# Kernel tuning notes

Measured on AMD Instinct MI355X. Metric: run time of the kernel, lower is better.

The kernel has to match this reference:

```python
import jax, jax.numpy as jnp
import numpy as np

V = 1000      # output_dim (vocab)
H = 512       # hidden_dim
D = 512       # input_dim == d_model of MHA
HEADS = 8
DK = D // HEADS
MEM = 512     # memory_len
BS = 128      # batch
TMAX = 160    # max decode steps (== max(output_lens))


def setup_inputs() -> dict:
    key = jax.random.key(0)
    ks = jax.random.split(key, 16)
    s = 0.05
    f = lambda k, shape: jax.random.normal(k, shape, jnp.float32) * s
    memory = jax.random.normal(ks[0], (MEM, BS, D), jnp.float32)
    lens = jnp.sort(jax.random.randint(ks[1], (BS,), 1, TMAX + 1))[::-1]
    lens = lens.at[0].set(TMAX)  # torch runs max(output_lens) steps; pin to TMAX
    return dict(
        memory=memory,
        emb=f(ks[2], (V, H)),
        Wq=f(ks[3], (D, 2 * H)), bq=f(ks[4], (D,)),
        Wk=f(ks[5], (D, D)), bk=f(ks[6], (D,)),
        Wv=f(ks[7], (D, D)), bv=f(ks[8], (D,)),
        W_ih=f(ks[9], (3 * H, D)), W_hh=f(ks[10], (3 * H, H)),
        b_ih=f(ks[11], (3 * H,)), b_hh=f(ks[12], (3 * H,)),
        Wfc=f(ks[13], (V, H)), bfc=f(ks[14], (V,)),
        output_lens=lens,
    )


def _forward(memory, emb, Wq, bq, Wk, bk, Wv, bv, W_ih, W_hh, b_ih, b_hh, Wfc, bfc, output_lens):
    mem_len, bs, _ = memory.shape
    scale = 1.0 / np.sqrt(DK)
    # Precompute key/value projections once (memory is constant over decode steps).
    # (mem_len, bs, D) -> (bs, heads, mem_len, dk)
    kp = (memory @ Wk.T + bk).reshape(mem_len, bs, HEADS, DK).transpose(1, 2, 0, 3)
    vp = (memory @ Wv.T + bv).reshape(mem_len, bs, HEADS, DK).transpose(1, 2, 0, 3)

    def step(carry, i):
        out, hid = carry  # (bs, V), (bs, H)
        tok = jnp.argmax(out, axis=-1)                 # greedy feedback (annotations=None)
        q = jnp.concatenate([emb[tok], hid], axis=-1) @ Wq.T + bq  # (bs, D)
        qh = q.reshape(bs, HEADS, DK)
        att = jax.nn.softmax(jnp.einsum('bhd,bhmd->bhm', qh, kp) * scale, axis=-1)
        ctx = jnp.einsum('bhm,bhmd->bhd', att, vp).reshape(bs, D)
        # GRU cell (PyTorch gate order: r, z, n)
        gi = ctx @ W_ih.T + b_ih
        gh = hid @ W_hh.T + b_hh
        ir, iz, inn = jnp.split(gi, 3, axis=-1)
        hr, hz, hn = jnp.split(gh, 3, axis=-1)
        r = jax.nn.sigmoid(ir + hr)
        z = jax.nn.sigmoid(iz + hz)
        n = jnp.tanh(inn + r * hn)
        h_new = (1.0 - z) * n + z * hid
        o_new = h_new @ Wfc.T + bfc
        # Ragged masking: torch truncates finished batch items; each item is
        # independent, so masking the recorded outputs is equivalent.
        run = (i < output_lens)[:, None]
        ys = (jnp.where(run, o_new, 0.0),
              jnp.where(run, h_new, 0.0),
              jnp.where(run, att.mean(axis=1), 0.0))
        return (o_new, h_new), ys

    init = (jnp.zeros((bs, V), jnp.float32), jnp.zeros((bs, H), jnp.float32))
    _, (outputs, hiddens, scores) = jax.lax.scan(step, init, jnp.arange(TMAX))
    return outputs, hiddens, scores  # (T,bs,V), (T,bs,H), (T,bs,mem_len)


def reference(memory, emb, Wq, bq, Wk, bk, Wv, bv, W_ih, W_hh, b_ih, b_hh, Wfc, bfc, output_lens):
    return _forward(memory, emb, Wq, bq, Wk, bk, Wv, bv, W_ih, W_hh, b_ih, b_hh, Wfc, bfc, output_lens)
```

## Files before the change

kernel.cpp:

```cpp
#include <hip/hip_runtime.h>
#include <math.h>

__global__ __launch_bounds__(256) void kv_proj(
    const float* __restrict__ mem, const float* __restrict__ W,
    const float* __restrict__ bias, float* __restrict__ outp) {
  __shared__ float As[32][68];
  __shared__ float Bs[32][68];
  int gid = blockIdx.x;
  int jt = gid & 7, mt = (gid >> 3) & 7, b = gid >> 6;
  int t = threadIdx.x;
  int lm = t >> 2;
  int kq = (t & 3) * 8;
  int tx = t & 15, ty = t >> 4;
  float acc[4][4];
  #pragma unroll
  for (int r = 0; r < 4; ++r)
    #pragma unroll
    for (int c = 0; c < 4; ++c) acc[r][c] = 0.f;
  const float* Arow = mem + (size_t)(mt * 64 + lm) * 65536 + (size_t)b * 512 + kq;
  const float* Brow = W + (size_t)(jt * 64 + lm) * 512 + kq;
  for (int k0 = 0; k0 < 512; k0 += 32) {
    float4 a0 = *(const float4*)(Arow + k0);
    float4 a1 = *(const float4*)(Arow + k0 + 4);
    float4 b0 = *(const float4*)(Brow + k0);
    float4 b1 = *(const float4*)(Brow + k0 + 4);
    As[kq + 0][lm] = a0.x; As[kq + 1][lm] = a0.y; As[kq + 2][lm] = a0.z; As[kq + 3][lm] = a0.w;
    As[kq + 4][lm] = a1.x; As[kq + 5][lm] = a1.y; As[kq + 6][lm] = a1.z; As[kq + 7][lm] = a1.w;
    Bs[kq + 0][lm] = b0.x; Bs[kq + 1][lm] = b0.y; Bs[kq + 2][lm] = b0.z; Bs[kq + 3][lm] = b0.w;
    Bs[kq + 4][lm] = b1.x; Bs[kq + 5][lm] = b1.y; Bs[kq + 6][lm] = b1.z; Bs[kq + 7][lm] = b1.w;
    __syncthreads();
    #pragma unroll
    for (int k = 0; k < 32; ++k) {
      float4 av = *(const float4*)&As[k][ty * 4];
      float4 bv = *(const float4*)&Bs[k][tx * 4];
      float ar[4] = {av.x, av.y, av.z, av.w};
      float br[4] = {bv.x, bv.y, bv.z, bv.w};
      #pragma unroll
      for (int r = 0; r < 4; ++r)
        #pragma unroll
        for (int c = 0; c < 4; ++c) acc[r][c] = fmaf(ar[r], br[c], acc[r][c]);
    }
    __syncthreads();
  }
  float4 bb = *(const float4*)(bias + jt * 64 + tx * 4);
  #pragma unroll
  for (int r = 0; r < 4; ++r) {
    int m = mt * 64 + ty * 4 + r;
    float4 o;
    o.x = acc[r][0] + bb.x; o.y = acc[r][1] + bb.y;
    o.z = acc[r][2] + bb.z; o.w = acc[r][3] + bb.w;
    *(float4*)(outp + (((size_t)b * 8 + jt) * 512 + m) * 64 + tx * 4) = o;
  }
}

__global__ __launch_bounds__(256) void kv_projT(
    const float* __restrict__ mem, const float* __restrict__ W,
    const float* __restrict__ bias, float* __restrict__ outp) {
  __shared__ float As[32][68];
  __shared__ float Bs[32][68];
  int gid = blockIdx.x;
  int jt = gid & 7, mt = (gid >> 3) & 7, b = gid >> 6;
  int t = threadIdx.x;
  int lm = t >> 2;
  int kq = (t & 3) * 8;
  int tx = t & 15, ty = t >> 4;
  float acc[4][4];
  #pragma unroll
  for (int r = 0; r < 4; ++r)
    #pragma unroll
    for (int c = 0; c < 4; ++c) acc[r][c] = 0.f;
  const float* Arow = mem + (size_t)(mt * 64 + lm) * 65536 + (size_t)b * 512 + kq;
  const float* Brow = W + (size_t)(jt * 64 + lm) * 512 + kq;
  for (int k0 = 0; k0 < 512; k0 += 32) {
    float4 a0 = *(const float4*)(Arow + k0);
    float4 a1 = *(const float4*)(Arow + k0 + 4);
    float4 b0 = *(const float4*)(Brow + k0);
    float4 b1 = *(const float4*)(Brow + k0 + 4);
    As[kq + 0][lm] = a0.x; As[kq + 1][lm] = a0.y; As[kq + 2][lm] = a0.z; As[kq + 3][lm] = a0.w;
    As[kq + 4][lm] = a1.x; As[kq + 5][lm] = a1.y; As[kq + 6][lm] = a1.z; As[kq + 7][lm] = a1.w;
    Bs[kq + 0][lm] = b0.x; Bs[kq + 1][lm] = b0.y; Bs[kq + 2][lm] = b0.z; Bs[kq + 3][lm] = b0.w;
    Bs[kq + 4][lm] = b1.x; Bs[kq + 5][lm] = b1.y; Bs[kq + 6][lm] = b1.z; Bs[kq + 7][lm] = b1.w;
    __syncthreads();
    #pragma unroll
    for (int k = 0; k < 32; ++k) {
      float4 av = *(const float4*)&As[k][ty * 4];
      float4 bv = *(const float4*)&Bs[k][tx * 4];
      float ar[4] = {av.x, av.y, av.z, av.w};
      float br[4] = {bv.x, bv.y, bv.z, bv.w};
      #pragma unroll
      for (int r = 0; r < 4; ++r)
        #pragma unroll
        for (int c = 0; c < 4; ++c) acc[r][c] = fmaf(ar[r], br[c], acc[r][c]);
    }
    __syncthreads();
  }
  float4 bb = *(const float4*)(bias + jt * 64 + tx * 4);
  float bc[4] = {bb.x, bb.y, bb.z, bb.w};
  #pragma unroll
  for (int r = 0; r < 4; ++r) {
    int m = mt * 64 + ty * 4 + r;
    #pragma unroll
    for (int c = 0; c < 4; ++c) {
      int d = tx * 4 + c;
      outp[((size_t)(b * 8 + jt) * 64 + d) * 512 + m] = acc[r][c] + bc[c];
    }
  }
}

__global__ __launch_bounds__(256) void init_kernel(float* __restrict__ h0,
                                                   unsigned long long* __restrict__ packed) {
  int t = threadIdx.x + blockIdx.x * blockDim.x;
  for (int i = t; i < 128 * 512; i += blockDim.x * gridDim.x) h0[i] = 0.f;
  if (t < 128) packed[t] = (0x80000000ull << 32) | 0xFFFFFFFFull;
}

__global__ __launch_bounds__(256) void attn_fused(
    const float* __restrict__ kpT, const float* __restrict__ vp,
    const float* __restrict__ emb, const float* __restrict__ Wq,
    const float* __restrict__ bq, const unsigned long long* __restrict__ packed,
    const float* __restrict__ h_prev, float* __restrict__ ctx,
    float* __restrict__ att_buf) {
  int b = blockIdx.x >> 3, hd = blockIdx.x & 7;
  __shared__ float act[1024];
  __shared__ float qs[64];
  __shared__ float att[512];
  __shared__ __align__(16) float red[16][68];
  __shared__ float rmax[4], rsum[4];
  __shared__ int tok_s;
  int t = threadIdx.x;
  if (t == 0) tok_s = (int)(0xFFFFFFFFu - (unsigned int)(packed[b] & 0xFFFFFFFFull));
  __syncthreads();
  int tok = tok_s;
  act[t]       = emb[(size_t)tok * 512 + t];
  act[256 + t] = emb[(size_t)tok * 512 + 256 + t];
  act[512 + t] = h_prev[(size_t)b * 512 + t];
  act[768 + t] = h_prev[(size_t)b * 512 + 256 + t];
  __syncthreads();

  {
    int jl = t >> 2, kc = t & 3;
    const float* wrow = Wq + (size_t)(hd * 64 + jl) * 1024 + kc * 256;
    const float* a = act + kc * 256;
    float p = 0.f;
    #pragma unroll 8
    for (int i = 0; i < 256; i += 4) {
      float4 w = *(const float4*)(wrow + i);
      p = fmaf(a[i + 0], w.x, p);
      p = fmaf(a[i + 1], w.y, p);
      p = fmaf(a[i + 2], w.z, p);
      p = fmaf(a[i + 3], w.w, p);
    }
    p += __shfl_xor(p, 1);
    p += __shfl_xor(p, 2);
    if (kc == 0) qs[jl] = p + bq[hd * 64 + jl];
  }
  __syncthreads();

  const float* Kb = kpT + (size_t)(b * 8 + hd) * 32768;
  float s0 = 0.f, s1 = 0.f;
  {
    int m2 = 2 * t;
    #pragma unroll 8
    for (int d = 0; d < 64; ++d) {
      float2 kk = *(const float2*)(Kb + (size_t)d * 512 + m2);
      float qd = qs[d];
      s0 = fmaf(qd, kk.x, s0);
      s1 = fmaf(qd, kk.y, s1);
    }
    s0 *= 0.125f;
    s1 *= 0.125f;
  }
  float mx = fmaxf(s0, s1);
  #pragma unroll
  for (int o = 32; o > 0; o >>= 1) mx = fmaxf(mx, __shfl_xor(mx, o));
  if ((t & 63) == 0) rmax[t >> 6] = mx;
  __syncthreads();
  mx = fmaxf(fmaxf(rmax[0], rmax[1]), fmaxf(rmax[2], rmax[3]));
  float e0 = expf(s0 - mx), e1 = expf(s1 - mx);
  float sm = e0 + e1;
  #pragma unroll
  for (int o = 32; o > 0; o >>= 1) sm += __shfl_xor(sm, o);
  if ((t & 63) == 0) rsum[t >> 6] = sm;
  __syncthreads();
  sm = rsum[0] + rsum[1] + rsum[2] + rsum[3];
  float inv = 1.f / sm;
  float a0 = e0 * inv, a1 = e1 * inv;
  att[2 * t] = a0;
  att[2 * t + 1] = a1;
  *(float2*)(att_buf + (size_t)(b * 8 + hd) * 512 + 2 * t) = make_float2(a0, a1);
  __syncthreads();

  const float* Vb = vp + (size_t)(b * 8 + hd) * 32768;
  {
    int dsl = (t & 15) * 4, g = t >> 4;
    float c0 = 0.f, c1 = 0.f, c2 = 0.f, c3 = 0.f;
    #pragma unroll 4
    for (int m = g; m < 512; m += 16) {
      float4 vv = *(const float4*)(Vb + (size_t)m * 64 + dsl);
      float am = att[m];
      c0 = fmaf(am, vv.x, c0);
      c1 = fmaf(am, vv.y, c1);
      c2 = fmaf(am, vv.z, c2);
      c3 = fmaf(am, vv.w, c3);
    }
    red[g][dsl + 0] = c0;
    red[g][dsl + 1] = c1;
    red[g][dsl + 2] = c2;
    red[g][dsl + 3] = c3;
  }
  __syncthreads();
  if (t < 64) {
    float cc = 0.f;
    #pragma unroll
    for (int g2 = 0; g2 < 16; ++g2) cc += red[g2][t];
    ctx[(size_t)b * 512 + hd * 64 + t] = cc;
  }
}

__global__ __launch_bounds__(256) void gru_kernel(
    const float* __restrict__ W_ih, const float* __restrict__ W_hh,
    const float* __restrict__ b_ih, const float* __restrict__ b_hh,
    const float* __restrict__ ctx, const float* __restrict__ h_prev,
    float* __restrict__ h_new, const float* __restrict__ att_buf,
    const int* __restrict__ lens, float* __restrict__ out_hid,
    float* __restrict__ out_sc, unsigned long long* __restrict__ packed,
    int step) {
  __shared__ float cs[8][512];
  __shared__ float hs[8][512];
  int bi = blockIdx.x;
  int t = threadIdx.x;
  if (bi >= 256) {
    int sb = bi - 256;
    if (sb == 0 && t < 128) packed[t] = 0ull;
    #pragma unroll
    for (int i = 0; i < 4; ++i) {
      int flat = sb * 1024 + i * 256 + t;
      int bb = flat >> 9, m = flat & 511;
      float sum = 0.f;
      #pragma unroll
      for (int h = 0; h < 8; ++h) sum += att_buf[(size_t)(bb * 8 + h) * 512 + m];
      float val = sum * 0.125f;
      out_sc[(size_t)step * 65536 + flat] = (step < lens[bb]) ? val : 0.f;
    }
    return;
  }
  int bt = bi >> 4, jt = bi & 15;
  #pragma unroll
  for (int i = 0; i < 16; ++i) {
    int flat = i * 256 + t;
    int lb = flat >> 9, k = flat & 511;
    cs[lb][k] = ctx[(size_t)(bt * 8 + lb) * 512 + k];
    hs[lb][k] = h_prev[(size_t)(bt * 8 + lb) * 512 + k];
  }
  __syncthreads();
  int lb = t >> 5, j = (jt << 5) + (t & 31);
  int b = bt * 8 + lb;
  float air = b_ih[j], aiz = b_ih[512 + j], ain = b_ih[1024 + j];
  float ahr = b_hh[j], ahz = b_hh[512 + j], ahn = b_hh[1024 + j];
  const float* c = cs[lb];
  const float* hh = hs[lb];
  const float* wi0 = W_ih + (size_t)j * 512;
  const float* wi1 = W_ih + (size_t)(512 + j) * 512;
  const float* wi2 = W_ih + (size_t)(1024 + j) * 512;
  const float* wh0 = W_hh + (size_t)j * 512;
  const float* wh1 = W_hh + (size_t)(512 + j) * 512;
  const float* wh2 = W_hh + (size_t)(1024 + j) * 512;
  #pragma unroll 2
  for (int k = 0; k < 512; k += 4) {
    float4 wa = *(const float4*)(wi0 + k);
    float4 wb = *(const float4*)(wi1 + k);
    float4 wc = *(const float4*)(wi2 + k);
    float4 wd = *(const float4*)(wh0 + k);
    float4 we = *(const float4*)(wh1 + k);
    float4 wf = *(const float4*)(wh2 + k);
    float c0 = c[k], c1 = c[k + 1], c2 = c[k + 2], c3 = c[k + 3];
    float h0 = hh[k], h1 = hh[k + 1], h2 = hh[k + 2], h3 = hh[k + 3];
    air = fmaf(c0, wa.x, air); air = fmaf(c1, wa.y, air); air = fmaf(c2, wa.z, air); air = fmaf(c3, wa.w, air);
    aiz = fmaf(c0, wb.x, aiz); aiz = fmaf(c1, wb.y, aiz); aiz = fmaf(c2, wb.z, aiz); aiz = fmaf(c3, wb.w, aiz);
    ain = fmaf(c0, wc.x, ain); ain = fmaf(c1, wc.y, ain); ain = fmaf(c2, wc.z, ain); ain = fmaf(c3, wc.w, ain);
    ahr = fmaf(h0, wd.x, ahr); ahr = fmaf(h1, wd.y, ahr); ahr = fmaf(h2, wd.z, ahr); ahr = fmaf(h3, wd.w, ahr);
    ahz = fmaf(h0, we.x, ahz); ahz = fmaf(h1, we.y, ahz); ahz = fmaf(h2, we.z, ahz); ahz = fmaf(h3, we.w, ahz);
    ahn = fmaf(h0, wf.x, ahn); ahn = fmaf(h1, wf.y, ahn); ahn = fmaf(h2, wf.z, ahn); ahn = fmaf(h3, wf.w, ahn);
  }
  float r = 1.f / (1.f + expf(-(air + ahr)));
  float z = 1.f / (1.f + expf(-(aiz + ahz)));
  float n = tanhf(fmaf(r, ahn, ain));
  float hp = hh[j];
  float hv = (1.f - z) * n + z * hp;
  h_new[(size_t)b * 512 + j] = hv;
  out_hid[(size_t)step * 65536 + (size_t)b * 512 + j] = (step < lens[b]) ? hv : 0.f;
}

__global__ __launch_bounds__(256) void logits_kernel(
    const float* __restrict__ Wfc, const float* __restrict__ bfc,
    const float* __restrict__ h_new, const int* __restrict__ lens,
    float* __restrict__ out_o, unsigned long long* __restrict__ packed,
    int step) {
  __shared__ float hs[8][512];
  int bi = blockIdx.x;
  int t = threadIdx.x;
  int bt = bi >> 4, vt = bi & 15;
  #pragma unroll
  for (int i = 0; i < 16; ++i) {
    int flat = i * 256 + t;
    int lb = flat >> 9, k = flat & 511;
    hs[lb][k] = h_new[(size_t)(bt * 8 + lb) * 512 + k];
  }
  __syncthreads();
  int lb = t >> 5, vv = t & 31;
  int b = bt * 8 + lb;
  const float* a = hs[lb];
  int run = step < lens[b];
  float bestv = -1e30f;
  int besti = 0;
  #pragma unroll
  for (int r = 0; r < 2; ++r) {
    int v = vt * 64 + r * 32 + vv;
    if (v < 1000) {
      float acc = bfc[v];
      const float* wrow = Wfc + (size_t)v * 512;
      #pragma unroll 4
      for (int k = 0; k < 512; k += 4) {
        float4 w = *(const float4*)(wrow + k);
        acc = fmaf(a[k + 0], w.x, acc);
        acc = fmaf(a[k + 1], w.y, acc);
        acc = fmaf(a[k + 2], w.z, acc);
        acc = fmaf(a[k + 3], w.w, acc);
      }
      out_o[(size_t)step * 128000 + (size_t)b * 1000 + v] = run ? acc : 0.f;
      if (acc > bestv) { bestv = acc; besti = v; }
    }
  }
  #pragma unroll
  for (int o = 16; o > 0; o >>= 1) {
    float ov = __shfl_xor(bestv, o);
    int oi = __shfl_xor(besti, o);
    if (ov > bestv || (ov == bestv && oi < besti)) { bestv = ov; besti = oi; }
  }
  if (vv == 0) {
    unsigned int fb = __float_as_uint(bestv);
    fb = (fb & 0x80000000u) ? ~fb : (fb | 0x80000000u);
    unsigned long long key =
        ((unsigned long long)fb << 32) | (unsigned long long)(0xFFFFFFFFu - (unsigned int)besti);
    atomicMax(packed + b, key);
  }
}

extern "C" void kernel_launch(void* const* d_in, const int* in_sizes, int n_in,
                              void* d_out, int out_size, void* d_ws, size_t ws_size,
                              hipStream_t stream) {
  const float* memory = (const float*)d_in[0];
  const float* emb    = (const float*)d_in[1];
  const float* Wq     = (const float*)d_in[2];
  const float* bq     = (const float*)d_in[3];
  const float* Wk     = (const float*)d_in[4];
  const float* bk     = (const float*)d_in[5];
  const float* Wv     = (const float*)d_in[6];
  const float* bv     = (const float*)d_in[7];
  const float* W_ih   = (const float*)d_in[8];
  const float* W_hh   = (const float*)d_in[9];
  const float* b_ih   = (const float*)d_in[10];
  const float* b_hh   = (const float*)d_in[11];
  const float* Wfc    = (const float*)d_in[12];
  const float* bfc    = (const float*)d_in[13];
  const int* lens     = (const int*)d_in[14];

  float* ws = (float*)d_ws;
  float* kpT     = ws;
  float* vp      = kpT + 33554432;
  float* ctx     = vp + 33554432;
  float* h0      = ctx + 65536;
  float* h1      = h0 + 65536;
  float* att_buf = h1 + 65536;
  unsigned long long* packed = (unsigned long long*)(att_buf + 524288);

  float* out   = (float*)d_out;
  float* out_o = out;
  float* out_h = out + 20480000;
  float* out_s = out_h + 10485760;

  kv_projT<<<8192, 256, 0, stream>>>(memory, Wk, bk, kpT);
  kv_proj<<<8192, 256, 0, stream>>>(memory, Wv, bv, vp);
  init_kernel<<<64, 256, 0, stream>>>(h0, packed);

  for (int t = 0; t < 160; ++t) {
    float* hp = (t & 1) ? h1 : h0;
    float* hn = (t & 1) ? h0 : h1;
    attn_fused<<<1024, 256, 0, stream>>>(kpT, vp, emb, Wq, bq, packed, hp, ctx, att_buf);
    gru_kernel<<<320, 256, 0, stream>>>(W_ih, W_hh, b_ih, b_hh, ctx, hp, hn,
                                        att_buf, lens, out_h, out_s, packed, t);
    logits_kernel<<<256, 256, 0, stream>>>(Wfc, bfc, hn, lens, out_o, packed, t);
  }
}
```

Measured before the change: 31.61 ms.

## Precompute embedding query projection table and move hidden query projection into logits kernel

Splits the query projection algebraically: the embedding half is precomputed once as a vocab-by-D table (emb @ Wq_emb^T), and the hidden half is computed by extra blocks in the logits kernel from the new hidden state, so attention only gathers and adds. The attention kernel now spreads the score dot product across two head-dim halves with float4 loads, and the GRU and logits kernels move to 512 threads that split K in halves and reduce with shuffles. This removes the per-step 1024-long Wq dot product from every attention block (which was duplicated across heads per batch) at the cost of an upfront table, a transposed Wq copy and more extra blocks per step.

```diff
diff --git a/kernel.cpp b/kernel.cpp
--- a/kernel.cpp
+++ b/kernel.cpp
@@ -107,90 +107,147 @@
   }
 }
 
+__global__ __launch_bounds__(256) void embq_proj(
+    const float* __restrict__ emb, const float* __restrict__ Wq,
+    float* __restrict__ outp) {
+  __shared__ float As[32][68];
+  __shared__ float Bs[32][68];
+  int gid = blockIdx.x;
+  int jt = gid & 7, vt = gid >> 3;
+  int t = threadIdx.x;
+  int lm = t >> 2;
+  int kq = (t & 3) * 8;
+  int tx = t & 15, ty = t >> 4;
+  float acc[4][4];
+  #pragma unroll
+  for (int r = 0; r < 4; ++r)
+    #pragma unroll
+    for (int c = 0; c < 4; ++c) acc[r][c] = 0.f;
+  int v = vt * 64 + lm;
+  bool va = v < 1000;
+  const float* Arow = emb + (size_t)(va ? v : 0) * 512 + kq;
+  const float* Brow = Wq + (size_t)(jt * 64 + lm) * 1024 + kq;
+  for (int k0 = 0; k0 < 512; k0 += 32) {
+    float4 a0 = va ? *(const float4*)(Arow + k0) : make_float4(0, 0, 0, 0);
+    float4 a1 = va ? *(const float4*)(Arow + k0 + 4) : make_float4(0, 0, 0, 0);
+    float4 b0 = *(const float4*)(Brow + k0);
+    float4 b1 = *(const float4*)(Brow + k0 + 4);
+    As[kq + 0][lm] = a0.x; As[kq + 1][lm] = a0.y; As[kq + 2][lm] = a0.z; As[kq + 3][lm] = a0.w;
+    As[kq + 4][lm] = a1.x; As[kq + 5][lm] = a1.y; As[kq + 6][lm] = a1.z; As[kq + 7][lm] = a1.w;
+    Bs[kq + 0][lm] = b0.x; Bs[kq + 1][lm] = b0.y; Bs[kq + 2][lm] = b0.z; Bs[kq + 3][lm] = b0.w;
+    Bs[kq + 4][lm] = b1.x; Bs[kq + 5][lm] = b1.y; Bs[kq + 6][lm] = b1.z; Bs[kq + 7][lm] = b1.w;
+    __syncthreads();
+    #pragma unroll
+    for (int k = 0; k < 32; ++k) {
+      float4 av = *(const float4*)&As[k][ty * 4];
+      float4 bv = *(const float4*)&Bs[k][tx * 4];
+      float ar[4] = {av.x, av.y, av.z, av.w};
+      float br[4] = {bv.x, bv.y, bv.z, bv.w};
+      #pragma unroll
+      for (int r = 0; r < 4; ++r)
+        #pragma unroll
+        for (int c = 0; c < 4; ++c) acc[r][c] = fmaf(ar[r], br[c], acc[r][c]);
+    }
+    __syncthreads();
+  }
+  #pragma unroll
+  for (int r = 0; r < 4; ++r) {
+    int v2 = vt * 64 + ty * 4 + r;
+    if (v2 < 1000) {
+      float4 o;
+      o.x = acc[r][0]; o.y = acc[r][1]; o.z = acc[r][2]; o.w = acc[r][3];
+      *(float4*)(outp + (size_t)v2 * 512 + jt * 64 + tx * 4) = o;
+    }
+  }
+}
+
+__global__ __launch_bounds__(256) void wqh_transpose(
+    const float* __restrict__ Wq, float* __restrict__ WqhT) {
+  int idx = blockIdx.x * 256 + threadIdx.x;
+  int k = idx >> 9, j = idx & 511;
+  WqhT[(size_t)k * 512 + j] = Wq[(size_t)j * 1024 + 512 + k];
+}
+
 __global__ __launch_bounds__(256) void init_kernel(float* __restrict__ h0,
+                                                   float* __restrict__ qh,
                                                    unsigned long long* __restrict__ packed) {
-  int t = threadIdx.x + blockIdx.x * blockDim.x;
-  for (int i = t; i < 128 * 512; i += blockDim.x * gridDim.x) h0[i] = 0.f;
+  int t = threadIdx.x + blockIdx.x * 256;
+  for (int i = t; i < 128 * 512; i += 256 * 64) { h0[i] = 0.f; qh[i] = 0.f; }
   if (t < 128) packed[t] = (0x80000000ull << 32) | 0xFFFFFFFFull;
 }
 
 __global__ __launch_bounds__(256) void attn_fused(
     const float* __restrict__ kpT, const float* __restrict__ vp,
-    const float* __restrict__ emb, const float* __restrict__ Wq,
-    const float* __restrict__ bq, const unsigned long long* __restrict__ packed,
-    const float* __restrict__ h_prev, float* __restrict__ ctx,
-    float* __restrict__ att_buf) {
+    const float* __restrict__ emb_q, const float* __restrict__ qhp,
+    const float* __restrict__ bq_p, const unsigned long long* __restrict__ packed,
+    float* __restrict__ ctx, float* __restrict__ att_buf) {
   int b = blockIdx.x >> 3, hd = blockIdx.x & 7;
-  __shared__ float act[1024];
   __shared__ float qs[64];
   __shared__ float att[512];
+  __shared__ __align__(16) float sp[128][4];
   __shared__ __align__(16) float red[16][68];
-  __shared__ float rmax[4], rsum[4];
+  __shared__ float rmax[2], rsum[2];
   __shared__ int tok_s;
   int t = threadIdx.x;
   if (t == 0) tok_s = (int)(0xFFFFFFFFu - (unsigned int)(packed[b] & 0xFFFFFFFFull));
   __syncthreads();
-  int tok = tok_s;
-  act[t]       = emb[(size_t)tok * 512 + t];
-  act[256 + t] = emb[(size_t)tok * 512 + 256 + t];
-  act[512 + t] = h_prev[(size_t)b * 512 + t];
-  act[768 + t] = h_prev[(size_t)b * 512 + 256 + t];
-  __syncthreads();
-
+  if (t < 64) {
+    qs[t] = emb_q[(size_t)tok_s * 512 + hd * 64 + t]
+          + qhp[(size_t)b * 512 + hd * 64 + t] + bq_p[hd * 64 + t];
+  }
+  __syncthreads();
+  const float* Kb = kpT + (size_t)(b * 8 + hd) * 32768;
+  const float* Vb = vp + (size_t)(b * 8 + hd) * 32768;
+  int mq = (t & 127) * 4, dh = t >> 7;
+  float s0 = 0.f, s1 = 0.f, s2 = 0.f, s3 = 0.f;
   {
-    int jl = t >> 2, kc = t & 3;
-    const float* wrow = Wq + (size_t)(hd * 64 + jl) * 1024 + kc * 256;
-    const float* a = act + kc * 256;
-    float p = 0.f;
+    const float* Kbd = Kb + (size_t)(dh * 32) * 512 + mq;
+    const float* qd0 = qs + dh * 32;
     #pragma unroll 8
-    for (int i = 0; i < 256; i += 4) {
-      float4 w = *(const float4*)(wrow + i);
-      p = fmaf(a[i + 0], w.x, p);
-      p = fmaf(a[i + 1], w.y, p);
-      p = fmaf(a[i + 2], w.z, p);
-      p = fmaf(a[i + 3], w.w, p);
-    }
-    p += __shfl_xor(p, 1);
-    p += __shfl_xor(p, 2);
-    if (kc == 0) qs[jl] = p + bq[hd * 64 + jl];
-  }
-  __syncthreads();
-
-  const float* Kb = kpT + (size_t)(b * 8 + hd) * 32768;
-  float s0 = 0.f, s1 = 0.f;
-  {
-    int m2 = 2 * t;
-    #pragma unroll 8
-    for (int d = 0; d < 64; ++d) {
-      float2 kk = *(const float2*)(Kb + (size_t)d * 512 + m2);
-      float qd = qs[d];
+    for (int dd = 0; dd < 32; ++dd) {
+      float4 kk = *(const float4*)(Kbd + (size_t)dd * 512);
+      float qd = qd0[dd];
       s0 = fmaf(qd, kk.x, s0);
       s1 = fmaf(qd, kk.y, s1);
-    }
-    s0 *= 0.125f;
-    s1 *= 0.125f;
-  }
-  float mx = fmaxf(s0, s1);
-  #pragma unroll
-  for (int o = 32; o > 0; o >>= 1) mx = fmaxf(mx, __shfl_xor(mx, o));
-  if ((t & 63) == 0) rmax[t >> 6] = mx;
-  __syncthreads();
-  mx = fmaxf(fmaxf(rmax[0], rmax[1]), fmaxf(rmax[2], rmax[3]));
-  float e0 = expf(s0 - mx), e1 = expf(s1 - mx);
-  float sm = e0 + e1;
-  #pragma unroll
-  for (int o = 32; o > 0; o >>= 1) sm += __shfl_xor(sm, o);
-  if ((t & 63) == 0) rsum[t >> 6] = sm;
-  __syncthreads();
-  sm = rsum[0] + rsum[1] + rsum[2] + rsum[3];
-  float inv = 1.f / sm;
-  float a0 = e0 * inv, a1 = e1 * inv;
-  att[2 * t] = a0;
-  att[2 * t + 1] = a1;
-  *(float2*)(att_buf + (size_t)(b * 8 + hd) * 512 + 2 * t) = make_float2(a0, a1);
-  __syncthreads();
-
-  const float* Vb = vp + (size_t)(b * 8 + hd) * 32768;
+      s2 = fmaf(qd, kk.z, s2);
+      s3 = fmaf(qd, kk.w, s3);
+    }
+  }
+  if (dh) {
+    sp[t & 127][0] = s0; sp[t & 127][1] = s1;
+    sp[t & 127][2] = s2; sp[t & 127][3] = s3;
+  }
+  __syncthreads();
+  float e0 = 0.f, e1 = 0.f, e2 = 0.f, e3 = 0.f;
+  if (!dh) {
+    s0 = (s0 + sp[t][0]) * 0.125f;
+    s1 = (s1 + sp[t][1]) * 0.125f;
+    s2 = (s2 + sp[t][2]) * 0.125f;
+    s3 = (s3 + sp[t][3]) * 0.125f;
+    float mx = fmaxf(fmaxf(s0, s1), fmaxf(s2, s3));
+    #pragma unroll
+    for (int o = 32; o > 0; o >>= 1) mx = fmaxf(mx, __shfl_xor(mx, o));
+    if ((t & 63) == 0) rmax[t >> 6] = mx;
+  }
+  __syncthreads();
+  if (!dh) {
+    float mx = fmaxf(rmax[0], rmax[1]);
+    e0 = expf(s0 - mx); e1 = expf(s1 - mx);
+    e2 = expf(s2 - mx); e3 = expf(s3 - mx);
+    float sm = e0 + e1 + e2 + e3;
+    #pragma unroll
+    for (int o = 32; o > 0; o >>= 1) sm += __shfl_xor(sm, o);
+    if ((t & 63) == 0) rsum[t >> 6] = sm;
+  }
+  __syncthreads();
+  if (!dh) {
+    float inv = 1.f / (rsum[0] + rsum[1]);
+    float4 a4;
+    a4.x = e0 * inv; a4.y = e1 * inv; a4.z = e2 * inv; a4.w = e3 * inv;
+    *(float4*)&att[mq] = a4;
+    *(float4*)(att_buf + (size_t)(b * 8 + hd) * 512 + mq) = a4;
+  }
+  __syncthreads();
   {
     int dsl = (t & 15) * 4, g = t >> 4;
     float c0 = 0.f, c1 = 0.f, c2 = 0.f, c3 = 0.f;
@@ -217,7 +274,7 @@
   }
 }
 
-__global__ __launch_bounds__(256) void gru_kernel(
+__global__ __launch_bounds__(512) void gru_kernel(
     const float* __restrict__ W_ih, const float* __restrict__ W_hh,
     const float* __restrict__ b_ih, const float* __restrict__ b_hh,
     const float* __restrict__ ctx, const float* __restrict__ h_prev,
@@ -233,40 +290,38 @@
     int sb = bi - 256;
     if (sb == 0 && t < 128) packed[t] = 0ull;
     #pragma unroll
-    for (int i = 0; i < 4; ++i) {
-      int flat = sb * 1024 + i * 256 + t;
+    for (int i = 0; i < 2; ++i) {
+      int flat = sb * 1024 + i * 512 + t;
       int bb = flat >> 9, m = flat & 511;
       float sum = 0.f;
       #pragma unroll
       for (int h = 0; h < 8; ++h) sum += att_buf[(size_t)(bb * 8 + h) * 512 + m];
-      float val = sum * 0.125f;
-      out_sc[(size_t)step * 65536 + flat] = (step < lens[bb]) ? val : 0.f;
+      out_sc[(size_t)step * 65536 + flat] = (step < lens[bb]) ? sum * 0.125f : 0.f;
     }
     return;
   }
   int bt = bi >> 4, jt = bi & 15;
   #pragma unroll
-  for (int i = 0; i < 16; ++i) {
-    int flat = i * 256 + t;
-    int lb = flat >> 9, k = flat & 511;
-    cs[lb][k] = ctx[(size_t)(bt * 8 + lb) * 512 + k];
-    hs[lb][k] = h_prev[(size_t)(bt * 8 + lb) * 512 + k];
-  }
-  __syncthreads();
-  int lb = t >> 5, j = (jt << 5) + (t & 31);
-  int b = bt * 8 + lb;
-  float air = b_ih[j], aiz = b_ih[512 + j], ain = b_ih[1024 + j];
-  float ahr = b_hh[j], ahz = b_hh[512 + j], ahn = b_hh[1024 + j];
-  const float* c = cs[lb];
-  const float* hh = hs[lb];
-  const float* wi0 = W_ih + (size_t)j * 512;
-  const float* wi1 = W_ih + (size_t)(512 + j) * 512;
-  const float* wi2 = W_ih + (size_t)(1024 + j) * 512;
-  const float* wh0 = W_hh + (size_t)j * 512;
-  const float* wh1 = W_hh + (size_t)(512 + j) * 512;
-  const float* wh2 = W_hh + (size_t)(1024 + j) * 512;
+  for (int i = 0; i < 8; ++i) {
+    int flat = i * 512 + t;
+    int lb2 = flat >> 9, k = flat & 511;
+    cs[lb2][k] = ctx[(size_t)(bt * 8 + lb2) * 512 + k];
+    hs[lb2][k] = h_prev[(size_t)(bt * 8 + lb2) * 512 + k];
+  }
+  __syncthreads();
+  int j5 = t & 31, kh = (t >> 5) & 1, lb = t >> 6;
+  int j = jt * 32 + j5, b = bt * 8 + lb, k0 = kh * 256;
+  const float* c = cs[lb] + k0;
+  const float* hh = hs[lb] + k0;
+  const float* wi0 = W_ih + (size_t)j * 512 + k0;
+  const float* wi1 = W_ih + (size_t)(512 + j) * 512 + k0;
+  const float* wi2 = W_ih + (size_t)(1024 + j) * 512 + k0;
+  const float* wh0 = W_hh + (size_t)j * 512 + k0;
+  const float* wh1 = W_hh + (size_t)(512 + j) * 512 + k0;
+  const float* wh2 = W_hh + (size_t)(1024 + j) * 512 + k0;
+  float air = 0.f, aiz = 0.f, ain = 0.f, ahr = 0.f, ahz = 0.f, ahn = 0.f;
   #pragma unroll 2
-  for (int k = 0; k < 512; k += 4) {
+  for (int k = 0; k < 256; k += 4) {
     float4 wa = *(const float4*)(wi0 + k);
     float4 wb = *(const float4*)(wi1 + k);
     float4 wc = *(const float4*)(wi2 + k);
@@ -282,53 +337,100 @@
     ahz = fmaf(h0, we.x, ahz); ahz = fmaf(h1, we.y, ahz); ahz = fmaf(h2, we.z, ahz); ahz = fmaf(h3, we.w, ahz);
     ahn = fmaf(h0, wf.x, ahn); ahn = fmaf(h1, wf.y, ahn); ahn = fmaf(h2, wf.z, ahn); ahn = fmaf(h3, wf.w, ahn);
   }
-  float r = 1.f / (1.f + expf(-(air + ahr)));
-  float z = 1.f / (1.f + expf(-(aiz + ahz)));
-  float n = tanhf(fmaf(r, ahn, ain));
-  float hp = hh[j];
-  float hv = (1.f - z) * n + z * hp;
-  h_new[(size_t)b * 512 + j] = hv;
-  out_hid[(size_t)step * 65536 + (size_t)b * 512 + j] = (step < lens[b]) ? hv : 0.f;
-}
-
-__global__ __launch_bounds__(256) void logits_kernel(
+  air += __shfl_xor(air, 32);
+  aiz += __shfl_xor(aiz, 32);
+  ain += __shfl_xor(ain, 32);
+  ahr += __shfl_xor(ahr, 32);
+  ahz += __shfl_xor(ahz, 32);
+  ahn += __shfl_xor(ahn, 32);
+  if (kh == 0) {
+    air += b_ih[j]; aiz += b_ih[512 + j]; ain += b_ih[1024 + j];
+    ahr += b_hh[j]; ahz += b_hh[512 + j]; ahn += b_hh[1024 + j];
+    float r = 1.f / (1.f + expf(-(air + ahr)));
+    float z = 1.f / (1.f + expf(-(aiz + ahz)));
+    float n = tanhf(fmaf(r, ahn, ain));
+    float hp = hs[lb][j];
+    float hv = (1.f - z) * n + z * hp;
+    h_new[(size_t)b * 512 + j] = hv;
+    out_hid[(size_t)step * 65536 + (size_t)b * 512 + j] = (step < lens[b]) ? hv : 0.f;
+  }
+}
+
+__global__ __launch_bounds__(512) void logits_kernel(
     const float* __restrict__ Wfc, const float* __restrict__ bfc,
     const float* __restrict__ h_new, const int* __restrict__ lens,
     float* __restrict__ out_o, unsigned long long* __restrict__ packed,
-    int step) {
+    const float* __restrict__ WqhT, float* __restrict__ qhp, int step) {
   __shared__ float hs[8][512];
+  __shared__ float hsb[512];
+  __shared__ float qpart[256][2];
   int bi = blockIdx.x;
   int t = threadIdx.x;
+  if (bi >= 256) {
+    int bb = bi - 256;
+    hsb[t & 511] = h_new[(size_t)bb * 512 + (t & 511)];
+    __syncthreads();
+    int j2 = t & 255, kh2 = t >> 8;
+    const float* wt = WqhT + (size_t)(kh2 * 256) * 512 + j2 * 2;
+    const float* hv2 = hsb + kh2 * 256;
+    float q0 = 0.f, q1 = 0.f;
+    #pragma unroll 8
+    for (int k = 0; k < 256; ++k) {
+      float2 w = *(const float2*)(wt + (size_t)k * 512);
+      float hk = hv2[k];
+      q0 = fmaf(hk, w.x, q0);
+      q1 = fmaf(hk, w.y, q1);
+    }
+    if (kh2) { qpart[j2][0] = q0; qpart[j2][1] = q1; }
+    __syncthreads();
+    if (!kh2) {
+      q0 += qpart[j2][0];
+      q1 += qpart[j2][1];
+      *(float2*)(qhp + (size_t)bb * 512 + j2 * 2) = make_float2(q0, q1);
+    }
+    return;
+  }
   int bt = bi >> 4, vt = bi & 15;
   #pragma unroll
-  for (int i = 0; i < 16; ++i) {
-    int flat = i * 256 + t;
-    int lb = flat >> 9, k = flat & 511;
-    hs[lb][k] = h_new[(size_t)(bt * 8 + lb) * 512 + k];
-  }
-  __syncthreads();
-  int lb = t >> 5, vv = t & 31;
-  int b = bt * 8 + lb;
-  const float* a = hs[lb];
-  int run = step < lens[b];
+  for (int i = 0; i < 8; ++i) {
+    int flat = i * 512 + t;
+    int lb2 = flat >> 9, k = flat & 511;
+    hs[lb2][k] = h_new[(size_t)(bt * 8 + lb2) * 512 + k];
+  }
+  __syncthreads();
+  int vv = t & 31, kh = (t >> 5) & 1, lb = t >> 6;
+  int b = bt * 8 + lb, k0 = kh * 256;
+  int v0 = vt * 64 + vv;
+  int v1 = vt * 64 + 32 + vv;
+  bool g1 = v1 < 1000;
+  const float* a = hs[lb] + k0;
+  const float* w0 = Wfc + (size_t)v0 * 512 + k0;
+  const float* w1 = Wfc + (size_t)(g1 ? v1 : v0) * 512 + k0;
+  float acc0 = 0.f, acc1 = 0.f;
+  #pragma unroll 2
+  for (int k = 0; k < 256; k += 4) {
+    float4 wA = *(const float4*)(w0 + k);
+    float4 wB = *(const float4*)(w1 + k);
+    float a0 = a[k], a1 = a[k + 1], a2 = a[k + 2], a3 = a[k + 3];
+    acc0 = fmaf(a0, wA.x, acc0); acc0 = fmaf(a1, wA.y, acc0);
+    acc0 = fmaf(a2, wA.z, acc0); acc0 = fmaf(a3, wA.w, acc0);
+    acc1 = fmaf(a0, wB.x, acc1); acc1 = fmaf(a1, wB.y, acc1);
+    acc1 = fmaf(a2, wB.z, acc1); acc1 = fmaf(a3, wB.w, acc1);
+  }
+  acc0 += __shfl_xor(acc0, 32);
+  acc1 += __shfl_xor(acc1, 32);
   float bestv = -1e30f;
   int besti = 0;
-  #pragma unroll
-  for (int r = 0; r < 2; ++r) {
-    int v = vt * 64 + r * 32 + vv;
-    if (v < 1000) {
-      float acc = bfc[v];
-      const float* wrow = Wfc + (size_t)v * 512;
-      #pragma unroll 4
-      for (int k = 0; k < 512; k += 4) {
-        float4 w = *(const float4*)(wrow + k);
-        acc = fmaf(a[k + 0], w.x, acc);
-        acc = fmaf(a[k + 1], w.y, acc);
-        acc = fmaf(a[k + 2], w.z, acc);
-        acc = fmaf(a[k + 3], w.w, acc);
-      }
-      out_o[(size_t)step * 128000 + (size_t)b * 1000 + v] = run ? acc : 0.f;
-      if (acc > bestv) { bestv = acc; besti = v; }
+  if (kh == 0) {
+    int run = step < lens[b];
+    size_t ofs = (size_t)step * 128000 + (size_t)b * 1000;
+    float f0 = acc0 + bfc[v0];
+    out_o[ofs + v0] = run ? f0 : 0.f;
+    bestv = f0; besti = v0;
+    if (g1) {
+      float f1 = acc1 + bfc[v1];
+      out_o[ofs + v1] = run ? f1 : 0.f;
+      if (f1 > bestv) { bestv = f1; besti = v1; }
     }
   }
   #pragma unroll
@@ -337,7 +439,7 @@
     int oi = __shfl_xor(besti, o);
     if (ov > bestv || (ov == bestv && oi < besti)) { bestv = ov; besti = oi; }
   }
-  if (vv == 0) {
+  if ((t & 63) == 0) {
     unsigned int fb = __float_as_uint(bestv);
     fb = (fb & 0x80000000u) ? ~fb : (fb | 0x80000000u);
     unsigned long long key =
@@ -372,7 +474,10 @@
   float* h0      = ctx + 65536;
   float* h1      = h0 + 65536;
   float* att_buf = h1 + 65536;
-  unsigned long long* packed = (unsigned long long*)(att_buf + 524288);
+  float* qh      = att_buf + 524288;
+  float* emb_q   = qh + 65536;
+  float* WqhT    = emb_q + 512000;
+  unsigned long long* packed = (unsigned long long*)(WqhT + 262144);
 
   float* out   = (float*)d_out;
   float* out_o = out;
@@ -381,14 +486,17 @@
 
   kv_projT<<<8192, 256, 0, stream>>>(memory, Wk, bk, kpT);
   kv_proj<<<8192, 256, 0, stream>>>(memory, Wv, bv, vp);
-  init_kernel<<<64, 256, 0, stream>>>(h0, packed);
+  embq_proj<<<128, 256, 0, stream>>>(emb, Wq, emb_q);
+  wqh_transpose<<<1024, 256, 0, stream>>>(Wq, WqhT);
+  init_kernel<<<64, 256, 0, stream>>>(h0, qh, packed);
 
   for (int t = 0; t < 160; ++t) {
     float* hp = (t & 1) ? h1 : h0;
     float* hn = (t & 1) ? h0 : h1;
-    attn_fused<<<1024, 256, 0, stream>>>(kpT, vp, emb, Wq, bq, packed, hp, ctx, att_buf);
-    gru_kernel<<<320, 256, 0, stream>>>(W_ih, W_hh, b_ih, b_hh, ctx, hp, hn,
+    attn_fused<<<1024, 256, 0, stream>>>(kpT, vp, emb_q, qh, bq, packed, ctx, att_buf);
+    gru_kernel<<<320, 512, 0, stream>>>(W_ih, W_hh, b_ih, b_hh, ctx, hp, hn,
                                         att_buf, lens, out_h, out_s, packed, t);
-    logits_kernel<<<256, 256, 0, stream>>>(Wfc, bfc, hn, lens, out_o, packed, t);
-  }
-}
+    logits_kernel<<<384, 512, 0, stream>>>(Wfc, bfc, hn, lens, out_o, packed,
+                                           WqhT, qh, t);
+  }
+}
```

Measured after the change: 33.58 ms. 6.2% more time.
